# Optimization experiments

Measured on AMD Instinct MI355X. Metric: run time of the kernel, lower is better.

The kernel has to match this reference:

```python
import jax, jax.numpy as jnp
import numpy as np

N = 100000
E = 1600000
B = 64
NUM_CLASSES = 10


def setup_inputs() -> dict:
    key = jax.random.key(0)
    ks = jax.random.split(key, 8)
    x = jax.random.normal(ks[0], (N, 5), dtype=jnp.float32)
    edge_index = jax.random.randint(ks[1], (2, E), 0, N, dtype=jnp.int64)
    batch = jnp.sort(jax.random.randint(ks[2], (N,), 0, B, dtype=jnp.int64))

    def glorot(k, fan_in, fan_out):
        s = jnp.sqrt(6.0 / (fan_in + fan_out)).astype(jnp.float32)
        return jax.random.uniform(k, (fan_in, fan_out), jnp.float32, -s, s)

    dims = [(5, 32), (32, 64), (64, 128), (128, 256)]
    Ws = [glorot(jax.random.fold_in(ks[3], i), a, b) for i, (a, b) in enumerate(dims)]
    bs = [jnp.zeros((b,), jnp.float32) for (_, b) in dims]
    fc1_w = glorot(ks[4], 256, 100)
    fc1_b = jnp.zeros((100,), jnp.float32)
    fc2_w = glorot(ks[5], 100, NUM_CLASSES)
    fc2_b = jnp.zeros((NUM_CLASSES,), jnp.float32)
    return {
        'x': x, 'edge_index': edge_index, 'batch': batch,
        'W1': Ws[0], 'b1': bs[0], 'W2': Ws[1], 'b2': bs[1],
        'W3': Ws[2], 'b3': bs[2], 'W4': Ws[3], 'b4': bs[3],
        'fc1_w': fc1_w, 'fc1_b': fc1_b, 'fc2_w': fc2_w, 'fc2_b': fc2_b,
    }


def _gcn_conv(x, W, b, src, dst, dinv):
    h = x @ W                                   # [N, out]
    norm = (dinv[src] * dinv[dst])[:, None]      # [E, 1]
    msg = h[src] * norm                          # gather + scale
    agg = jax.ops.segment_sum(msg, dst, num_segments=N)
    agg = agg + h * (dinv * dinv)[:, None]       # self-loop contribution
    return agg + b


def reference(x, edge_index, batch, W1, b1, W2, b2, W3, b3, W4, b4,
              fc1_w, fc1_b, fc2_w, fc2_b):
    src, dst = edge_index[0], edge_index[1]
    # degree including self-loop
    deg = jax.ops.segment_sum(jnp.ones((E,), jnp.float32), dst, num_segments=N) + 1.0
    dinv = jax.lax.rsqrt(deg)

    h = jax.nn.relu(_gcn_conv(x, W1, b1, src, dst, dinv))
    # mesh_unpool with pool target 0 -> identity
    h = jax.nn.relu(_gcn_conv(h, W2, b2, src, dst, dinv))
    h = jax.nn.relu(_gcn_conv(h, W3, b3, src, dst, dinv))
    h = jax.nn.relu(_gcn_conv(h, W4, b4, src, dst, dinv))

    # global mean pool over graphs
    sums = jax.ops.segment_sum(h, batch, num_segments=B)
    cnt = jax.ops.segment_sum(jnp.ones((N,), jnp.float32), batch, num_segments=B)
    pooled = sums / jnp.maximum(cnt, 1.0)[:, None]

    h = jax.nn.relu(pooled @ fc1_w + fc1_b)
    return jax.nn.log_softmax(h @ fc2_w + fc2_b, axis=-1)
```

## Files before the change

### kernel.cpp

```cpp
#include <hip/hip_runtime.h>
#include <hip/hip_bf16.h>
#include <cmath>

#define NN 100000
#define NE 1600000
#define NBATCH 64
#define NB 391
#define NBP 512
#define BCAP 5120
#define NPAD (NB * BCAP)

typedef __attribute__((ext_vector_type(8))) _Float16 f16x8;
typedef __attribute__((ext_vector_type(4))) float f32x4;

__device__ __forceinline__ void atomAdd(float* p, float v) {
  unsafeAtomicAdd(p, v);
}

__global__ __launch_bounds__(256) void k_bin(const int* __restrict__ src,
    const int* __restrict__ dst, int* __restrict__ bucketCnt, uint2* __restrict__ pairs,
    const float* __restrict__ W2, const float* __restrict__ W3, const float* __restrict__ W4,
    _Float16* __restrict__ Wt2, _Float16* __restrict__ Wt3, _Float16* __restrict__ Wt4) {
  __shared__ int hist[NBP];
  __shared__ int scn[NBP];
  __shared__ int ofs[NBP];
  __shared__ int gbase[NBP];
  __shared__ uint2 buf[4096];
  const int base = blockIdx.x * 4096;
  const int n = (NE - base < 4096) ? NE - base : 4096;
  for (int i = threadIdx.x; i < NBP; i += 256) hist[i] = 0;
  __syncthreads();

  int myS[16], myD[16];
  int nloc = 0;
  for (int i = threadIdx.x, j = 0; i < n; i += 256, ++j) {
    myS[j] = src[base + i];
    myD[j] = dst[base + i];
    atomicAdd(&hist[myD[j] >> 8], 1);
    nloc = j + 1;
  }
  __syncthreads();

  scn[threadIdx.x] = hist[threadIdx.x];
  scn[threadIdx.x + 256] = hist[threadIdx.x + 256];
  __syncthreads();
  for (int off = 1; off < NBP; off <<= 1) {
    const int i0 = threadIdx.x, i1 = threadIdx.x + 256;
    int t0 = (i0 >= off) ? scn[i0 - off] : 0;
    int t1 = (i1 >= off) ? scn[i1 - off] : 0;
    __syncthreads();
    scn[i0] += t0;
    scn[i1] += t1;
    __syncthreads();
  }
  ofs[threadIdx.x] = scn[threadIdx.x] - hist[threadIdx.x];
  ofs[threadIdx.x + 256] = scn[threadIdx.x + 256] - hist[threadIdx.x + 256];
  for (int b = threadIdx.x; b < NB; b += 256) {
    int c = hist[b];
    if (c) gbase[b] = b * BCAP + atomicAdd(&bucketCnt[b], c);
  }
  __syncthreads();

  for (int j = 0; j < nloc; ++j) {
    int b = myD[j] >> 8;
    int slot = atomicAdd(&ofs[b], 1);
    buf[slot] = make_uint2((unsigned)myS[j], (unsigned)myD[j]);
  }
  __syncthreads();

  for (int i = threadIdx.x; i < n; i += 256) {
    uint2 p = buf[i];
    int b = (int)(p.y >> 8);
    int ex = scn[b] - hist[b];
    pairs[gbase[b] + (i - ex)] = p;
  }

  int idx = blockIdx.x * 256 + threadIdx.x;
  if (idx < 2048) {
    int k = idx / 64, m = idx - k * 64;
    Wt2[m * 32 + k] = (_Float16)W2[idx];
  } else if (idx < 10240) {
    int j = idx - 2048;
    int k = j / 128, m = j - k * 128;
    Wt3[m * 64 + k] = (_Float16)W3[j];
  } else if (idx < 43008) {
    int j = idx - 10240;
    int k = j / 256, m = j - k * 256;
    Wt4[m * 128 + k] = (_Float16)W4[j];
  }
}

__global__ __launch_bounds__(256) void k_cntfill(const uint2* __restrict__ pairs,
    const int* __restrict__ bucketCnt, const int* __restrict__ batch,
    const float* __restrict__ x, int* __restrict__ rowbeg, int* __restrict__ rowend,
    float* __restrict__ dinv, int* __restrict__ csrc, float* __restrict__ pcnt,
    _Float16* __restrict__ xs8) {
  __shared__ int c[256];
  __shared__ int scn[256];
  __shared__ int rowb[256];
  __shared__ int ofs[256];
  __shared__ int h[64];
  const int tid = threadIdx.x;
  c[tid] = 0; ofs[tid] = 0;
  if (tid < 64) h[tid] = 0;
  __syncthreads();
  const int b = blockIdx.x;
  const int s = b * BCAP;
  const int e = s + bucketCnt[b];
  for (int i = s + tid; i < e; i += 256) atomicAdd(&c[pairs[i].y & 255], 1);
  __syncthreads();
  const int v = c[tid];
  scn[tid] = v;
  __syncthreads();
  for (int off = 1; off < 256; off <<= 1) {
    int t = (tid >= off) ? scn[tid - off] : 0;
    __syncthreads();
    scn[tid] += t;
    __syncthreads();
  }
  rowb[tid] = s + scn[tid] - v;
  const int node = b * 256 + tid;
  rowbeg[node] = rowb[tid];
  rowend[node] = rowb[tid] + v;
  if (node < NN) {
    const float di = rsqrtf((float)v + 1.0f);
    dinv[node] = di;
    f16x8 o = {0, 0, 0, 0, 0, 0, 0, 0};
    o[0] = (_Float16)(x[(size_t)node * 5 + 0] * di);
    o[1] = (_Float16)(x[(size_t)node * 5 + 1] * di);
    o[2] = (_Float16)(x[(size_t)node * 5 + 2] * di);
    o[3] = (_Float16)(x[(size_t)node * 5 + 3] * di);
    o[4] = (_Float16)(x[(size_t)node * 5 + 4] * di);
    *(f16x8*)(xs8 + (size_t)node * 8) = o;
    atomicAdd(&h[batch[node]], 1);
  }
  __syncthreads();
  for (int i = s + tid; i < e; i += 256) {
    uint2 p = pairs[i];
    int t = (int)(p.y & 255);
    int pos = rowb[t] + atomicAdd(&ofs[t], 1);
    csrc[pos] = (int)p.x;
  }
  if (tid < 64 && h[tid]) atomAdd(&pcnt[tid], (float)h[tid]);
}

__global__ __launch_bounds__(256) void k_l1v(const _Float16* __restrict__ xs8,
    const int* __restrict__ rowbeg, const int* __restrict__ rowend,
    const int* __restrict__ csrc, const float* __restrict__ dinv,
    const float* __restrict__ W, const float* __restrict__ b,
    _Float16* __restrict__ outp) {
  __shared__ float w_s[160];
  __shared__ float b_s[32];
  const int tid = threadIdx.x;
  if (tid < 160) w_s[tid] = W[tid];
  if (tid < 32) b_s[tid] = b[tid];
  __syncthreads();
  const int r = blockIdx.x * 256 + tid;
  if (r >= NN) return;
  const float di = dinv[r];
  f16x8 a = *(const f16x8*)(xs8 + (size_t)r * 8);
  f16x8 cacc = {0, 0, 0, 0, 0, 0, 0, 0};
  int e = rowbeg[r];
  const int e1 = rowend[r];
  for (; e + 2 <= e1; e += 2) {
    const int s0 = csrc[e], s1 = csrc[e + 1];
    a    += *(const f16x8*)(xs8 + (size_t)s0 * 8);
    cacc += *(const f16x8*)(xs8 + (size_t)s1 * 8);
  }
  if (e < e1) a += *(const f16x8*)(xs8 + (size_t)csrc[e] * 8);
  a += cacc;
  const float f0 = (float)a[0] * di, f1 = (float)a[1] * di, f2 = (float)a[2] * di,
              f3 = (float)a[3] * di, f4 = (float)a[4] * di;
  _Float16 ov[32];
#pragma unroll
  for (int j = 0; j < 32; ++j) {
    float s = b_s[j] + f0 * w_s[j] + f1 * w_s[32 + j] + f2 * w_s[64 + j]
                     + f3 * w_s[96 + j] + f4 * w_s[128 + j];
    ov[j] = (_Float16)(fmaxf(s, 0.f) * di);
  }
  uint4* op = (uint4*)(outp + (size_t)r * 32);
  op[0] = *(uint4*)&ov[0];
  op[1] = *(uint4*)&ov[8];
  op[2] = *(uint4*)&ov[16];
  op[3] = *(uint4*)&ov[24];
}

template<int K>
__global__ __launch_bounds__(256) void k_gatherb(const _Float16* __restrict__ in,
    const int* __restrict__ rowbeg, const int* __restrict__ rowend,
    const int* __restrict__ csrc, const float* __restrict__ dinv,
    _Float16* __restrict__ agg) {
  constexpr int TPR = K / 8;
  constexpr int RPB = 256 / TPR;
  const int r = blockIdx.x * RPB + threadIdx.x / TPR;
  if (r >= NN) return;
  const int c = (threadIdx.x % TPR) * 8;
  const float di = dinv[r];
  f16x8 a0 = *(const f16x8*)(in + (size_t)r * K + c);
  f16x8 a1 = {0, 0, 0, 0, 0, 0, 0, 0};
  f16x8 a2 = {0, 0, 0, 0, 0, 0, 0, 0};
  f16x8 a3 = {0, 0, 0, 0, 0, 0, 0, 0};
  int e = rowbeg[r];
  const int e1 = rowend[r];
  for (; e + 8 <= e1; e += 8) {
    const int s0 = csrc[e],     s1 = csrc[e + 1], s2 = csrc[e + 2], s3 = csrc[e + 3];
    const int s4 = csrc[e + 4], s5 = csrc[e + 5], s6 = csrc[e + 6], s7 = csrc[e + 7];
    const f16x8 v0 = *(const f16x8*)(in + (size_t)s0 * K + c);
    const f16x8 v1 = *(const f16x8*)(in + (size_t)s1 * K + c);
    const f16x8 v2 = *(const f16x8*)(in + (size_t)s2 * K + c);
    const f16x8 v3 = *(const f16x8*)(in + (size_t)s3 * K + c);
    const f16x8 v4 = *(const f16x8*)(in + (size_t)s4 * K + c);
    const f16x8 v5 = *(const f16x8*)(in + (size_t)s5 * K + c);
    const f16x8 v6 = *(const f16x8*)(in + (size_t)s6 * K + c);
    const f16x8 v7 = *(const f16x8*)(in + (size_t)s7 * K + c);
    a0 += v0; a1 += v1; a2 += v2; a3 += v3;
    a0 += v4; a1 += v5; a2 += v6; a3 += v7;
  }
  for (; e + 2 <= e1; e += 2) {
    const int s0 = csrc[e], s1 = csrc[e + 1];
    a0 += *(const f16x8*)(in + (size_t)s0 * K + c);
    a1 += *(const f16x8*)(in + (size_t)s1 * K + c);
  }
  if (e < e1) a0 += *(const f16x8*)(in + (size_t)csrc[e] * K + c);
  a0 = (a0 + a1) + (a2 + a3);
  const _Float16 dh = (_Float16)di;
  const f16x8 ds = {dh, dh, dh, dh, dh, dh, dh, dh};
  a0 *= ds;
  *(f16x8*)(agg + (size_t)r * K + c) = a0;
}

template<int K, int M, int MODE>
__global__ __launch_bounds__(256) void k_gemm_mfma(const _Float16* __restrict__ agg,
    const _Float16* __restrict__ Wt, const float* __restrict__ bias,
    const float* __restrict__ dinv, _Float16* __restrict__ outp,
    const int* __restrict__ batch, float* __restrict__ pooled) {
  constexpr int KP = K + 8;
  constexpr int KC = 32;
  constexpr int WP = KC + 8;
  constexpr int CTW = M / 64;
  constexpr int C8 = K / 8;
  __shared__ _Float16 a_s[64 * KP];
  __shared__ _Float16 w_s[M * WP];
  const int r0 = blockIdx.x * 64;
  const int tid = threadIdx.x;

  for (int idx = tid; idx < 64 * C8; idx += 256) {
    int row = idx / C8, cc = (idx % C8) * 8;
    uint4 v = {0u, 0u, 0u, 0u};
    if (r0 + row < NN) v = *(const uint4*)(agg + (size_t)(r0 + row) * K + cc);
    *(uint4*)&a_s[row * KP + cc] = v;
  }

  const int wave = tid >> 6, lane = tid & 63;
  const int m16 = lane & 15, q = lane >> 4;
  f32x4 acc[4][CTW];
#pragma unroll
  for (int rt = 0; rt < 4; ++rt)
#pragma unroll
    for (int ct = 0; ct < CTW; ++ct) acc[rt][ct] = (f32x4){0.f, 0.f, 0.f, 0.f};

  for (int kc = 0; kc < K; kc += KC) {
    __syncthreads();
    for (int idx = tid; idx < M * (KC / 8); idx += 256) {
      int m = idx / (KC / 8), cc = (idx % (KC / 8)) * 8;
      uint4 v = *(const uint4*)(Wt + (size_t)m * K + kc + cc);
      *(uint4*)&w_s[m * WP + cc] = v;
    }
    __syncthreads();
    f16x8 bfr[CTW];
#pragma unroll
    for (int ct = 0; ct < CTW; ++ct)
      bfr[ct] = *(const f16x8*)&w_s[(wave * (M / 4) + ct * 16 + m16) * WP + q * 8];
#pragma unroll
    for (int rt = 0; rt < 4; ++rt) {
      f16x8 afr = *(const f16x8*)&a_s[(rt * 16 + m16) * KP + kc + q * 8];
#pragma unroll
      for (int ct = 0; ct < CTW; ++ct)
        acc[rt][ct] = __builtin_amdgcn_mfma_f32_16x16x32_f16(afr, bfr[ct], acc[rt][ct], 0, 0, 0);
    }
  }

  if constexpr (MODE == 1) {
    const int rlast = (r0 + 63 < NN) ? r0 + 63 : NN - 1;
    const int bmin = batch[r0];
    const int bmax = batch[rlast];
    int rowb[4][4];
#pragma unroll
    for (int rt = 0; rt < 4; ++rt)
#pragma unroll
      for (int reg = 0; reg < 4; ++reg) {
        const int row = r0 + rt * 16 + q * 4 + reg;
        rowb[rt][reg] = (row < NN) ? batch[row] : -1;
      }
#pragma unroll
    for (int ct = 0; ct < CTW; ++ct) {
      const int col = wave * (M / 4) + ct * 16 + m16;
      const float bv = bias[col];
      for (int b = bmin; b <= bmax; ++b) {
        float s = 0.f;
#pragma unroll
        for (int rt = 0; rt < 4; ++rt)
#pragma unroll
          for (int reg = 0; reg < 4; ++reg)
            if (rowb[rt][reg] == b) s += fmaxf(acc[rt][ct][reg] + bv, 0.f);
        s += __shfl_xor(s, 16);
        s += __shfl_xor(s, 32);
        if (q == 0) atomAdd(&pooled[b * M + col], s);
      }
    }
  } else {
    float dsc[4][4];
#pragma unroll
    for (int rt = 0; rt < 4; ++rt)
#pragma unroll
      for (int reg = 0; reg < 4; ++reg) {
        const int row = r0 + rt * 16 + q * 4 + reg;
        dsc[rt][reg] = (row < NN) ? dinv[row] : 0.f;
      }
#pragma unroll
    for (int rt = 0; rt < 4; ++rt) {
#pragma unroll
      for (int ct = 0; ct < CTW; ++ct) {
        const int col = wave * (M / 4) + ct * 16 + m16;
        const float bv = bias[col];
#pragma unroll
        for (int reg = 0; reg < 4; ++reg) {
          const int row = r0 + rt * 16 + q * 4 + reg;
          if (row < NN) {
            float vv = fmaxf(acc[rt][ct][reg] + bv, 0.f) * dsc[rt][reg];
            outp[(size_t)row * M + col] = (_Float16)vv;
          }
        }
      }
    }
  }
}

__global__ __launch_bounds__(128) void k_mlp(const float* __restrict__ pooled,
    const float* __restrict__ cnt, const float* __restrict__ w1,
    const float* __restrict__ b1, const float* __restrict__ w2,
    const float* __restrict__ b2, float* __restrict__ out) {
  __shared__ float p[256];
  __shared__ float h1[100];
  __shared__ float lo[10];
  const int b = blockIdx.x;
  const float inv = 1.0f / fmaxf(cnt[b], 1.0f);
  for (int i = threadIdx.x; i < 256; i += 128) p[i] = pooled[b * 256 + i] * inv;
  __syncthreads();
  for (int j = threadIdx.x; j < 100; j += 128) {
    float s = b1[j];
    for (int k = 0; k < 256; ++k) s += p[k] * w1[k * 100 + j];
    h1[j] = fmaxf(s, 0.f);
  }
  __syncthreads();
  if (threadIdx.x < 10) {
    int j = threadIdx.x;
    float s = b2[j];
    for (int k = 0; k < 100; ++k) s += h1[k] * w2[k * 10 + j];
    lo[j] = s;
  }
  __syncthreads();
  if (threadIdx.x == 0) {
    float m = lo[0];
    for (int j = 1; j < 10; ++j) m = fmaxf(m, lo[j]);
    float ssum = 0.f;
    for (int j = 0; j < 10; ++j) ssum += expf(lo[j] - m);
    float lse = m + logf(ssum);
    for (int j = 0; j < 10; ++j) out[b * 10 + j] = lo[j] - lse;
  }
}

extern "C" void kernel_launch(void* const* d_in, const int* in_sizes, int n_in,
                              void* d_out, int out_size, void* d_ws, size_t ws_size,
                              hipStream_t stream) {
  const float* x     = (const float*)d_in[0];
  const int*   ei    = (const int*)d_in[1];
  const int*   batch = (const int*)d_in[2];
  const float* W1 = (const float*)d_in[3];  const float* b1 = (const float*)d_in[4];
  const float* W2 = (const float*)d_in[5];  const float* b2 = (const float*)d_in[6];
  const float* W3 = (const float*)d_in[7];  const float* b3 = (const float*)d_in[8];
  const float* W4 = (const float*)d_in[9];  const float* b4 = (const float*)d_in[10];
  const float* fc1w = (const float*)d_in[11]; const float* fc1b = (const float*)d_in[12];
  const float* fc2w = (const float*)d_in[13]; const float* fc2b = (const float*)d_in[14];
  float* out = (float*)d_out;

  const int* src = ei;
  const int* dst = ei + NE;

  float* ws = (float*)d_ws;
  float* pooled = ws;
  float* pcnt   = pooled + 16384;
  int*   bucketCnt = (int*)(pcnt + 64);
  float* dinv   = (float*)(bucketCnt + 512);
  int*   rowbeg = (int*)(dinv + 100352);
  int*   rowend = rowbeg + 100352;
  int*   csrc   = rowend + 100352;
  uint2* pairs  = (uint2*)(csrc + NPAD);
  _Float16* xs8 = (_Float16*)(pairs + NPAD);
  _Float16* F0  = xs8 + 800768;
  _Float16* F1  = F0 + (size_t)NN * 32;
  _Float16* F2  = F1 + (size_t)NN * 64;
  _Float16* AG  = F2 + (size_t)NN * 128;
  _Float16* Wt2 = AG + (size_t)NN * 128;
  _Float16* Wt3 = Wt2 + 32 * 64;
  _Float16* Wt4 = Wt3 + 64 * 128;

  (void)hipMemsetAsync(pooled, 0, (16384 + 64 + 512) * sizeof(float), stream);
  k_bin<<<(NE + 4095) / 4096, 256, 0, stream>>>(src, dst, bucketCnt, pairs,
                                                W2, W3, W4, Wt2, Wt3, Wt4);
  k_cntfill<<<NB, 256, 0, stream>>>(pairs, bucketCnt, batch, x,
                                    rowbeg, rowend, dinv, csrc, pcnt, xs8);

  k_l1v<<<(NN + 255) / 256, 256, 0, stream>>>(xs8, rowbeg, rowend, csrc, dinv, W1, b1, F0);

  k_gatherb<32><<<(NN + 63) / 64, 256, 0, stream>>>(F0, rowbeg, rowend, csrc, dinv, AG);
  k_gemm_mfma<32, 64, 0><<<(NN + 63) / 64, 256, 0, stream>>>(
      AG, Wt2, b2, dinv, F1, nullptr, nullptr);

  k_gatherb<64><<<(NN + 31) / 32, 256, 0, stream>>>(F1, rowbeg, rowend, csrc, dinv, AG);
  k_gemm_mfma<64, 128, 0><<<(NN + 63) / 64, 256, 0, stream>>>(
      AG, Wt3, b3, dinv, F2, nullptr, nullptr);

  k_gatherb<128><<<(NN + 15) / 16, 256, 0, stream>>>(F2, rowbeg, rowend, csrc, dinv, AG);
  k_gemm_mfma<128, 256, 1><<<(NN + 63) / 64, 256, 0, stream>>>(
      AG, Wt4, b4, dinv, nullptr, batch, pooled);

  k_mlp<<<NBATCH, 128, 0, stream>>>(pooled, pcnt, fc1w, fc1b, fc2w, fc2b, out);
}
```

Measured before the change: 318.7 us.

## Store layer 2/3 features in FP8 and pack edge pairs into 32 bits

Intermediate features F1 and F2 are now stored as FP8 (e4m3 via the hardware pack-convert) rather than FP16. New gather kernels read 16 FP8 values per thread, convert them to fp32, accumulate in fp32, and write FP16 aggregates for the MFMA GEMM. The binning step packs src<<8 | dst-low-byte into one 32-bit word, halving pair traffic, and the FP16 gather loop is also narrowed from 8 to 4 edges per iteration. The aim is to cut memory bandwidth in the edge-gather stages. The cost is lower numerical precision, and the packing assumes source indices fit in 24 bits.

```diff
diff --git a/kernel.cpp b/kernel.cpp
--- a/kernel.cpp
+++ b/kernel.cpp
@@ -12,20 +12,27 @@
 
 typedef __attribute__((ext_vector_type(8))) _Float16 f16x8;
 typedef __attribute__((ext_vector_type(4))) float f32x4;
+typedef __attribute__((ext_vector_type(2))) float f32x2;
 
 __device__ __forceinline__ void atomAdd(float* p, float v) {
   unsafeAtomicAdd(p, v);
 }
 
+__device__ __forceinline__ unsigned char f2fp8(float f) {
+  int pk = __builtin_amdgcn_cvt_pk_fp8_f32(f, f, 0, false);
+  return (unsigned char)(pk & 0xff);
+}
+
 __global__ __launch_bounds__(256) void k_bin(const int* __restrict__ src,
-    const int* __restrict__ dst, int* __restrict__ bucketCnt, uint2* __restrict__ pairs,
+    const int* __restrict__ dst, int* __restrict__ bucketCnt, unsigned* __restrict__ pairs,
     const float* __restrict__ W2, const float* __restrict__ W3, const float* __restrict__ W4,
     _Float16* __restrict__ Wt2, _Float16* __restrict__ Wt3, _Float16* __restrict__ Wt4) {
   __shared__ int hist[NBP];
   __shared__ int scn[NBP];
   __shared__ int ofs[NBP];
   __shared__ int gbase[NBP];
-  __shared__ uint2 buf[4096];
+  __shared__ unsigned buf[4096];
+  __shared__ unsigned short bufb[4096];
   const int base = blockIdx.x * 4096;
   const int n = (NE - base < 4096) ? NE - base : 4096;
   for (int i = threadIdx.x; i < NBP; i += 256) hist[i] = 0;
@@ -64,15 +71,15 @@
   for (int j = 0; j < nloc; ++j) {
     int b = myD[j] >> 8;
     int slot = atomicAdd(&ofs[b], 1);
-    buf[slot] = make_uint2((unsigned)myS[j], (unsigned)myD[j]);
+    buf[slot] = ((unsigned)myS[j] << 8) | ((unsigned)myD[j] & 255u);
+    bufb[slot] = (unsigned short)b;
   }
   __syncthreads();
 
   for (int i = threadIdx.x; i < n; i += 256) {
-    uint2 p = buf[i];
-    int b = (int)(p.y >> 8);
+    int b = (int)bufb[i];
     int ex = scn[b] - hist[b];
-    pairs[gbase[b] + (i - ex)] = p;
+    pairs[gbase[b] + (i - ex)] = buf[i];
   }
 
   int idx = blockIdx.x * 256 + threadIdx.x;
@@ -90,7 +97,7 @@
   }
 }
 
-__global__ __launch_bounds__(256) void k_cntfill(const uint2* __restrict__ pairs,
+__global__ __launch_bounds__(256) void k_cntfill(const unsigned* __restrict__ pairs,
     const int* __restrict__ bucketCnt, const int* __restrict__ batch,
     const float* __restrict__ x, int* __restrict__ rowbeg, int* __restrict__ rowend,
     float* __restrict__ dinv, int* __restrict__ csrc, float* __restrict__ pcnt,
@@ -107,7 +114,7 @@
   const int b = blockIdx.x;
   const int s = b * BCAP;
   const int e = s + bucketCnt[b];
-  for (int i = s + tid; i < e; i += 256) atomicAdd(&c[pairs[i].y & 255], 1);
+  for (int i = s + tid; i < e; i += 256) atomicAdd(&c[pairs[i] & 255u], 1);
   __syncthreads();
   const int v = c[tid];
   scn[tid] = v;
@@ -136,10 +143,10 @@
   }
   __syncthreads();
   for (int i = s + tid; i < e; i += 256) {
-    uint2 p = pairs[i];
-    int t = (int)(p.y & 255);
+    unsigned p = pairs[i];
+    int t = (int)(p & 255u);
     int pos = rowb[t] + atomicAdd(&ofs[t], 1);
-    csrc[pos] = (int)p.x;
+    csrc[pos] = (int)(p >> 8);
   }
   if (tid < 64 && h[tid]) atomAdd(&pcnt[tid], (float)h[tid]);
 }
@@ -202,26 +209,14 @@
   f16x8 a3 = {0, 0, 0, 0, 0, 0, 0, 0};
   int e = rowbeg[r];
   const int e1 = rowend[r];
-  for (; e + 8 <= e1; e += 8) {
-    const int s0 = csrc[e],     s1 = csrc[e + 1], s2 = csrc[e + 2], s3 = csrc[e + 3];
-    const int s4 = csrc[e + 4], s5 = csrc[e + 5], s6 = csrc[e + 6], s7 = csrc[e + 7];
-    const f16x8 v0 = *(const f16x8*)(in + (size_t)s0 * K + c);
-    const f16x8 v1 = *(const f16x8*)(in + (size_t)s1 * K + c);
-    const f16x8 v2 = *(const f16x8*)(in + (size_t)s2 * K + c);
-    const f16x8 v3 = *(const f16x8*)(in + (size_t)s3 * K + c);
-    const f16x8 v4 = *(const f16x8*)(in + (size_t)s4 * K + c);
-    const f16x8 v5 = *(const f16x8*)(in + (size_t)s5 * K + c);
-    const f16x8 v6 = *(const f16x8*)(in + (size_t)s6 * K + c);
-    const f16x8 v7 = *(const f16x8*)(in + (size_t)s7 * K + c);
-    a0 += v0; a1 += v1; a2 += v2; a3 += v3;
-    a0 += v4; a1 += v5; a2 += v6; a3 += v7;
-  }
-  for (; e + 2 <= e1; e += 2) {
-    const int s0 = csrc[e], s1 = csrc[e + 1];
+  for (; e + 4 <= e1; e += 4) {
+    const int s0 = csrc[e], s1 = csrc[e + 1], s2 = csrc[e + 2], s3 = csrc[e + 3];
     a0 += *(const f16x8*)(in + (size_t)s0 * K + c);
     a1 += *(const f16x8*)(in + (size_t)s1 * K + c);
-  }
-  if (e < e1) a0 += *(const f16x8*)(in + (size_t)csrc[e] * K + c);
+    a2 += *(const f16x8*)(in + (size_t)s2 * K + c);
+    a3 += *(const f16x8*)(in + (size_t)s3 * K + c);
+  }
+  for (; e < e1; ++e) a0 += *(const f16x8*)(in + (size_t)csrc[e] * K + c);
   a0 = (a0 + a1) + (a2 + a3);
   const _Float16 dh = (_Float16)di;
   const f16x8 ds = {dh, dh, dh, dh, dh, dh, dh, dh};
@@ -229,10 +224,78 @@
   *(f16x8*)(agg + (size_t)r * K + c) = a0;
 }
 
+template<int K>
+__global__ __launch_bounds__(256) void k_gather8(const unsigned char* __restrict__ in,
+    const int* __restrict__ rowbeg, const int* __restrict__ rowend,
+    const int* __restrict__ csrc, const float* __restrict__ dinv,
+    _Float16* __restrict__ agg) {
+  constexpr int TPR = K / 16;
+  constexpr int RPB = 256 / TPR;
+  const int r = blockIdx.x * RPB + threadIdx.x / TPR;
+  if (r >= NN) return;
+  const int c = (threadIdx.x % TPR) * 16;
+  const float di = dinv[r];
+  f32x2 acc[8];
+  {
+    const uint4 v = *(const uint4*)(in + (size_t)r * K + c);
+    acc[0] = __builtin_amdgcn_cvt_pk_f32_fp8(v.x, false);
+    acc[1] = __builtin_amdgcn_cvt_pk_f32_fp8(v.x, true);
+    acc[2] = __builtin_amdgcn_cvt_pk_f32_fp8(v.y, false);
+    acc[3] = __builtin_amdgcn_cvt_pk_f32_fp8(v.y, true);
+    acc[4] = __builtin_amdgcn_cvt_pk_f32_fp8(v.z, false);
+    acc[5] = __builtin_amdgcn_cvt_pk_f32_fp8(v.z, true);
+    acc[6] = __builtin_amdgcn_cvt_pk_f32_fp8(v.w, false);
+    acc[7] = __builtin_amdgcn_cvt_pk_f32_fp8(v.w, true);
+  }
+  int e = rowbeg[r];
+  const int e1 = rowend[r];
+  for (; e + 2 <= e1; e += 2) {
+    const int s0 = csrc[e], s1 = csrc[e + 1];
+    const uint4 v0 = *(const uint4*)(in + (size_t)s0 * K + c);
+    const uint4 v1 = *(const uint4*)(in + (size_t)s1 * K + c);
+    acc[0] += __builtin_amdgcn_cvt_pk_f32_fp8(v0.x, false);
+    acc[1] += __builtin_amdgcn_cvt_pk_f32_fp8(v0.x, true);
+    acc[2] += __builtin_amdgcn_cvt_pk_f32_fp8(v0.y, false);
+    acc[3] += __builtin_amdgcn_cvt_pk_f32_fp8(v0.y, true);
+    acc[4] += __builtin_amdgcn_cvt_pk_f32_fp8(v0.z, false);
+    acc[5] += __builtin_amdgcn_cvt_pk_f32_fp8(v0.z, true);
+    acc[6] += __builtin_amdgcn_cvt_pk_f32_fp8(v0.w, false);
+    acc[7] += __builtin_amdgcn_cvt_pk_f32_fp8(v0.w, true);
+    acc[0] += __builtin_amdgcn_cvt_pk_f32_fp8(v1.x, false);
+    acc[1] += __builtin_amdgcn_cvt_pk_f32_fp8(v1.x, true);
+    acc[2] += __builtin_amdgcn_cvt_pk_f32_fp8(v1.y, false);
+    acc[3] += __builtin_amdgcn_cvt_pk_f32_fp8(v1.y, true);
+    acc[4] += __builtin_amdgcn_cvt_pk_f32_fp8(v1.z, false);
+    acc[5] += __builtin_amdgcn_cvt_pk_f32_fp8(v1.z, true);
+    acc[6] += __builtin_amdgcn_cvt_pk_f32_fp8(v1.w, false);
+    acc[7] += __builtin_amdgcn_cvt_pk_f32_fp8(v1.w, true);
+  }
+  if (e < e1) {
+    const uint4 v0 = *(const uint4*)(in + (size_t)csrc[e] * K + c);
+    acc[0] += __builtin_amdgcn_cvt_pk_f32_fp8(v0.x, false);
+    acc[1] += __builtin_amdgcn_cvt_pk_f32_fp8(v0.x, true);
+    acc[2] += __builtin_amdgcn_cvt_pk_f32_fp8(v0.y, false);
+    acc[3] += __builtin_amdgcn_cvt_pk_f32_fp8(v0.y, true);
+    acc[4] += __builtin_amdgcn_cvt_pk_f32_fp8(v0.z, false);
+    acc[5] += __builtin_amdgcn_cvt_pk_f32_fp8(v0.z, true);
+    acc[6] += __builtin_amdgcn_cvt_pk_f32_fp8(v0.w, false);
+    acc[7] += __builtin_amdgcn_cvt_pk_f32_fp8(v0.w, true);
+  }
+  _Float16 o[16];
+#pragma unroll
+  for (int j = 0; j < 8; ++j) {
+    o[2 * j]     = (_Float16)(acc[j].x * di);
+    o[2 * j + 1] = (_Float16)(acc[j].y * di);
+  }
+  uint4* op = (uint4*)(agg + (size_t)r * K + c);
+  op[0] = *(uint4*)&o[0];
+  op[1] = *(uint4*)&o[8];
+}
+
 template<int K, int M, int MODE>
 __global__ __launch_bounds__(256) void k_gemm_mfma(const _Float16* __restrict__ agg,
     const _Float16* __restrict__ Wt, const float* __restrict__ bias,
-    const float* __restrict__ dinv, _Float16* __restrict__ outp,
+    const float* __restrict__ dinv, void* __restrict__ outp,
     const int* __restrict__ batch, float* __restrict__ pooled) {
   constexpr int KP = K + 8;
   constexpr int KC = 32;
@@ -281,6 +344,7 @@
   }
 
   if constexpr (MODE == 1) {
+    float* pl = (float*)pooled;
     const int rlast = (r0 + 63 < NN) ? r0 + 63 : NN - 1;
     const int bmin = batch[r0];
     const int bmax = batch[rlast];
@@ -305,10 +369,11 @@
             if (rowb[rt][reg] == b) s += fmaxf(acc[rt][ct][reg] + bv, 0.f);
         s += __shfl_xor(s, 16);
         s += __shfl_xor(s, 32);
-        if (q == 0) atomAdd(&pooled[b * M + col], s);
+        if (q == 0) atomAdd(&pl[b * M + col], s);
       }
     }
   } else {
+    unsigned char* out8 = (unsigned char*)outp;
     float dsc[4][4];
 #pragma unroll
     for (int rt = 0; rt < 4; ++rt)
@@ -328,7 +393,7 @@
           const int row = r0 + rt * 16 + q * 4 + reg;
           if (row < NN) {
             float vv = fmaxf(acc[rt][ct][reg] + bv, 0.f) * dsc[rt][reg];
-            outp[(size_t)row * M + col] = (_Float16)vv;
+            out8[(size_t)row * M + col] = f2fp8(vv);
           }
         }
       }
@@ -395,12 +460,12 @@
   int*   rowbeg = (int*)(dinv + 100352);
   int*   rowend = rowbeg + 100352;
   int*   csrc   = rowend + 100352;
-  uint2* pairs  = (uint2*)(csrc + NPAD);
+  unsigned* pairs = (unsigned*)(csrc + NPAD);
   _Float16* xs8 = (_Float16*)(pairs + NPAD);
   _Float16* F0  = xs8 + 800768;
-  _Float16* F1  = F0 + (size_t)NN * 32;
-  _Float16* F2  = F1 + (size_t)NN * 64;
-  _Float16* AG  = F2 + (size_t)NN * 128;
+  unsigned char* F1 = (unsigned char*)(F0 + (size_t)NN * 32);
+  unsigned char* F2 = F1 + (size_t)NN * 64;
+  _Float16* AG  = (_Float16*)(F2 + (size_t)NN * 128);
   _Float16* Wt2 = AG + (size_t)NN * 128;
   _Float16* Wt3 = Wt2 + 32 * 64;
   _Float16* Wt4 = Wt3 + 64 * 128;
@@ -417,11 +482,11 @@
   k_gemm_mfma<32, 64, 0><<<(NN + 63) / 64, 256, 0, stream>>>(
       AG, Wt2, b2, dinv, F1, nullptr, nullptr);
 
-  k_gatherb<64><<<(NN + 31) / 32, 256, 0, stream>>>(F1, rowbeg, rowend, csrc, dinv, AG);
+  k_gather8<64><<<(NN + 63) / 64, 256, 0, stream>>>(F1, rowbeg, rowend, csrc, dinv, AG);
   k_gemm_mfma<64, 128, 0><<<(NN + 63) / 64, 256, 0, stream>>>(
       AG, Wt3, b3, dinv, F2, nullptr, nullptr);
 
-  k_gatherb<128><<<(NN + 15) / 16, 256, 0, stream>>>(F2, rowbeg, rowend, csrc, dinv, AG);
+  k_gather8<128><<<(NN + 31) / 32, 256, 0, stream>>>(F2, rowbeg, rowend, csrc, dinv, AG);
   k_gemm_mfma<128, 256, 1><<<(NN + 63) / 64, 256, 0, stream>>>(
       AG, Wt4, b4, dinv, nullptr, batch, pooled);
 
```

New measurement: 293.6 us. 1.09x faster.
